# Performance work log

Measured on AMD Instinct MI355X. Metric: run time of the kernel, lower is better.

Reference implementation:

```python
import jax, jax.numpy as jnp
import numpy as np

B, DIN, DOUT, NW = 32768, 768, 768, 48
NH = NW // 3  # num_haar == num_mexican == num_morlet == 16 for NW=48
OMEGA0 = 5.0
LN_EPS = 1e-5


def setup_inputs() -> dict:
    key = jax.random.key(0)
    ks = jax.random.split(key, 6)
    x = jax.random.normal(ks[0], (B, DIN), dtype=jnp.float32)
    # kaiming-normal-ish fan_in init for linear layers, zero bias
    W = jax.random.normal(ks[1], (DOUT, DIN), dtype=jnp.float32) / np.sqrt(DIN)
    b = jnp.zeros((DOUT,), jnp.float32)
    Wp = jax.random.normal(ks[2], (NW, DIN), dtype=jnp.float32) / np.sqrt(DIN)
    bp = jnp.zeros((NW,), jnp.float32)
    Wc = jax.random.normal(ks[3], (DOUT, NW), dtype=jnp.float32) / np.sqrt(NW)
    bc = jnp.zeros((DOUT,), jnp.float32)
    # mixed-type init: per-family logspace scales / linspace translations
    scales = jnp.asarray(np.concatenate([
        np.logspace(-0.5, 0.5, NH),
        np.logspace(-0.3, 0.7, NH),
        np.logspace(-0.3, 0.7, NW - 2 * NH)]), jnp.float32)
    translations = jnp.asarray(np.concatenate([
        np.linspace(-1.5, 1.5, NH),
        np.linspace(-1.5, 1.5, NH),
        np.linspace(-1.5, 1.5, NW - 2 * NH)]), jnp.float32)
    gamma = jnp.ones((DOUT,), jnp.float32)
    beta = jnp.zeros((DOUT,), jnp.float32)
    return {"x": x, "W": W, "b": b, "Wp": Wp, "bp": bp, "Wc": Wc,
            "bc": bc, "scales": scales, "translations": translations,
            "gamma": gamma, "beta": beta}


def _wavelet_basis(s):
    # s: [B, NW] already scaled/translated; columns split by family
    dt = s.dtype
    sh = s[:, :NH]
    haar = (((sh >= 0) & (sh < 0.5)).astype(dt)
            - ((sh >= 0.5) & (sh < 1.0)).astype(dt))
    sm = s[:, NH:2 * NH]
    mexican = (1.0 - sm * sm) * jnp.exp(-0.5 * sm * sm)
    so = s[:, 2 * NH:]
    morlet = jnp.cos(OMEGA0 * so) * jnp.exp(-0.5 * so * so)
    return jnp.concatenate([haar, mexican, morlet], axis=1)


def reference(x, W, b, Wp, bp, Wc, bc, scales, translations, gamma, beta):
    direct = x @ W.T + b                              # [B, DOUT]
    wi = x @ Wp.T + bp                                # [B, NW]
    s = (wi - translations) / scales                  # [B, NW]
    wav = jax.nn.gelu(_wavelet_basis(s), approximate=False)
    wpath = wav @ Wc.T + bc                           # [B, DOUT]
    h = direct + wpath
    mu = jnp.mean(h, axis=-1, keepdims=True)
    var = jnp.mean((h - mu) ** 2, axis=-1, keepdims=True)
    return (h - mu) * jax.lax.rsqrt(var + LN_EPS) * gamma + beta
```

## Files before the change

kernel.cpp:

```cpp
#include <hip/hip_runtime.h>
#include <math.h>


#define B_SZ  32768
#define DIN   768
#define DOUT  768
#define NWAV  48

#define WF_OFF   0
#define WPH_OFF  589824
#define WPL_OFF  638976
#define WCF_OFF  688128

typedef short bf16x8 __attribute__((ext_vector_type(8)));
typedef float f32x16 __attribute__((ext_vector_type(16)));

__device__ __forceinline__ float bf2f(short u) {
    union { unsigned int i; float f; } v;
    v.i = ((unsigned int)(unsigned short)u) << 16;
    return v.f;
}
__device__ __forceinline__ short f2bf(float f) {
    union { float f; unsigned int i; } v; v.f = f;
    unsigned int r = v.i + 0x7FFFu + ((v.i >> 16) & 1u);
    return (short)(r >> 16);
}

__global__ __launch_bounds__(256) void pack_kernel(
    const float* __restrict__ W, const float* __restrict__ Wp,
    const float* __restrict__ Wc, short* __restrict__ ws)
{
    const int gw = (blockIdx.x * 256 + threadIdx.x) >> 6;
    const int L  = threadIdx.x & 63;
    const int lm = L & 31, half = L >> 5;

    if (gw < 1152) {
        const int cb = gw / 48, kb = gw % 48;
        const int row = cb * 32 + lm;
        const int k = kb * 16 + half * 8;
        bf16x8 o;
#pragma unroll
        for (int j = 0; j < 8; j++) o[j] = f2bf(W[(size_t)row * DIN + k + j]);
        *reinterpret_cast<bf16x8*>(&ws[WF_OFF + (size_t)gw * 512 + L * 8]) = o;
    } else if (gw < 1248) {
        const int t = gw - 1152;
        const int ct = t / 48, kb = t % 48;
        const int j = ct * 32 + lm;
        const int k = kb * 16 + half * 8;
        bf16x8 h, l;
#pragma unroll
        for (int jj = 0; jj < 8; jj++) {
            float v = (j < NWAV) ? Wp[(size_t)j * DIN + k + jj] : 0.f;
            const short hh = f2bf(v);
            h[jj] = hh;
            l[jj] = f2bf(v - bf2f(hh));
        }
        *reinterpret_cast<bf16x8*>(&ws[WPH_OFF + (size_t)t * 512 + L * 8]) = h;
        *reinterpret_cast<bf16x8*>(&ws[WPL_OFF + (size_t)t * 512 + L * 8]) = l;
    } else if (gw < 1320) {
        const int t = gw - 1248;
        const int cb = t / 3, kb = t % 3;
        const int row = cb * 32 + lm;
        const int k = kb * 16 + half * 8;
        bf16x8 o;
#pragma unroll
        for (int jj = 0; jj < 8; jj++) o[jj] = f2bf(Wc[(size_t)row * NWAV + k + jj]);
        *reinterpret_cast<bf16x8*>(&ws[WCF_OFF + (size_t)t * 512 + L * 8]) = o;
    }
}

__global__ __launch_bounds__(1024) void fused_kernel(
    const float* __restrict__ x, const short* __restrict__ ws,
    const float* __restrict__ Wp,
    const float* __restrict__ bp, const float* __restrict__ sc,
    const float* __restrict__ tr,
    const float* __restrict__ bb, const float* __restrict__ bc,
    const float* __restrict__ gm, const float* __restrict__ bt,
    float* __restrict__ out)
{
    __shared__ __align__(16) short xbuf[73728];
    __shared__ __align__(16) short wavL[64 * 72];
    __shared__ float redS[64 * 8], redQ[64 * 8];
    __shared__ float muA[64], rsA[64];

    short (*xh)[64 * 72] = reinterpret_cast<short (*)[64 * 72]>(&xbuf[0]);
    short (*xl)[64 * 72] = reinterpret_cast<short (*)[64 * 72]>(&xbuf[2 * 64 * 72]);
    float* wiS = reinterpret_cast<float*>(&xbuf[0]);

    const short* WF  = ws + WF_OFF;
    const short* WPH = ws + WPH_OFF;
    const short* WPL = ws + WPL_OFF;
    const short* WCF = ws + WCF_OFF;

    const int tid = threadIdx.x;
    const int r0  = blockIdx.x * 64;
    const int wv  = tid >> 6, L = tid & 63;
    const int lm  = L & 31, half = L >> 5;
    const int rg  = wv >> 3, cg = wv & 7;
    const int kq  = wv >> 2;
    const int wrg = (wv & 3) >> 1, wch = wv & 1;

    f32x16 acc[3];
#pragma unroll
    for (int ct = 0; ct < 3; ct++)
#pragma unroll
        for (int g = 0; g < 16; g++) acc[ct][g] = 0.f;
    f32x16 wacc;
#pragma unroll
    for (int g = 0; g < 16; g++) wacc[g] = 0.f;

    const int srow = tid >> 4;
    const int skc  = (tid & 15) * 4;

    {
        const float4 v = *reinterpret_cast<const float4*>(&x[(size_t)(r0 + srow) * DIN + skc]);
        const float f[4] = {v.x, v.y, v.z, v.w};
        short hh[4], ll[4];
#pragma unroll
        for (int i = 0; i < 4; i++) {
            hh[i] = f2bf(f[i]);
            ll[i] = f2bf(f[i] - bf2f(hh[i]));
        }
        *reinterpret_cast<short4*>(&xh[0][srow * 72 + skc]) = *reinterpret_cast<short4*>(hh);
        *reinterpret_cast<short4*>(&xl[0][srow * 72 + skc]) = *reinterpret_cast<short4*>(ll);
    }
    __syncthreads();

    for (int k0i = 0; k0i < 12; ++k0i) {
        const int cur = k0i & 1;
        float4 pf;
        if (k0i < 11)
            pf = *reinterpret_cast<const float4*>(&x[(size_t)(r0 + srow) * DIN + (k0i + 1) * 64 + skc]);

        const int kb0 = k0i * 4;
#pragma unroll
        for (int ks = 0; ks < 4; ++ks) {
            const bf16x8 a0 = *reinterpret_cast<bf16x8*>(&xh[cur][(rg * 32 + lm) * 72 + ks * 16 + half * 8]);
#pragma unroll
            for (int ct = 0; ct < 3; ++ct) {
                const bf16x8 b = *reinterpret_cast<const bf16x8*>(
                    &WF[((size_t)((cg * 3 + ct) * 48 + kb0 + ks)) * 512 + L * 8]);
                acc[ct] = __builtin_amdgcn_mfma_f32_32x32x16_bf16(a0, b, acc[ct], 0, 0, 0);
            }
        }
        if (k0i >= kq * 3 && k0i < kq * 3 + 3) {
#pragma unroll
            for (int ks = 0; ks < 4; ++ks) {
                const bf16x8 ah = *reinterpret_cast<bf16x8*>(&xh[cur][(wrg * 32 + lm) * 72 + ks * 16 + half * 8]);
                const bf16x8 al = *reinterpret_cast<bf16x8*>(&xl[cur][(wrg * 32 + lm) * 72 + ks * 16 + half * 8]);
                const bf16x8 bh = *reinterpret_cast<const bf16x8*>(
                    &WPH[((size_t)(wch * 48 + kb0 + ks)) * 512 + L * 8]);
                const bf16x8 bl = *reinterpret_cast<const bf16x8*>(
                    &WPL[((size_t)(wch * 48 + kb0 + ks)) * 512 + L * 8]);
                wacc = __builtin_amdgcn_mfma_f32_32x32x16_bf16(ah, bl, wacc, 0, 0, 0);
                wacc = __builtin_amdgcn_mfma_f32_32x32x16_bf16(al, bh, wacc, 0, 0, 0);
                wacc = __builtin_amdgcn_mfma_f32_32x32x16_bf16(ah, bh, wacc, 0, 0, 0);
            }
        }
        if (k0i < 11) {
            const float f[4] = {pf.x, pf.y, pf.z, pf.w};
            short hh[4], ll[4];
#pragma unroll
            for (int i = 0; i < 4; i++) {
                hh[i] = f2bf(f[i]);
                ll[i] = f2bf(f[i] - bf2f(hh[i]));
            }
            *reinterpret_cast<short4*>(&xh[1 - cur][srow * 72 + skc]) = *reinterpret_cast<short4*>(hh);
            *reinterpret_cast<short4*>(&xl[1 - cur][srow * 72 + skc]) = *reinterpret_cast<short4*>(ll);
        }
        __syncthreads();
    }

    if (kq < 2) {
#pragma unroll
        for (int g = 0; g < 16; ++g) {
            const int row = wrg * 32 + (g & 3) + 8 * (g >> 2) + 4 * half;
            wiS[(size_t)kq * 4096 + row * 64 + wch * 32 + lm] = wacc[g];
        }
    }
    __syncthreads();
    if (kq >= 2) {
#pragma unroll
        for (int g = 0; g < 16; ++g) {
            const int row = wrg * 32 + (g & 3) + 8 * (g >> 2) + 4 * half;
            wiS[(size_t)(kq - 2) * 4096 + row * 64 + wch * 32 + lm] += wacc[g];
        }
    }
    __syncthreads();

    const int j = L;
    if (j < NWAV) {
        const float bpv = bp[j], scv = sc[j], trv = tr[j];
#pragma unroll
        for (int rr = 0; rr < 4; ++rr) {
            const int row = wv * 4 + rr;
            const float wi = wiS[row * 64 + j] + wiS[4096 + row * 64 + j] + bpv;
            const float s = (wi - trv) / scv;
            float w;
            if (j < 16) {
                const float dmin = fminf(fabsf(s), fminf(fabsf(s - 0.5f), fabsf(s - 1.0f)));
                if (dmin < 2e-4f) {
                    const float* xr = &x[(size_t)(r0 + row) * DIN];
                    const float* wr = &Wp[(size_t)j * DIN];
                    double a0 = 0.0, a1 = 0.0, a2 = 0.0, a3 = 0.0;
                    for (int k = 0; k < DIN; k += 4) {
                        a0 = fma((double)xr[k + 0], (double)wr[k + 0], a0);
                        a1 = fma((double)xr[k + 1], (double)wr[k + 1], a1);
                        a2 = fma((double)xr[k + 2], (double)wr[k + 2], a2);
                        a3 = fma((double)xr[k + 3], (double)wr[k + 3], a3);
                    }
                    const double wid = ((a0 + a1) + (a2 + a3)) + (double)bpv;
                    const double sd = (wid - (double)trv) / (double)scv;
                    w = (sd >= 0.0 && sd < 0.5) ? 1.f : ((sd >= 0.5 && sd < 1.0) ? -1.f : 0.f);
                } else {
                    w = (s >= 0.f && s < 0.5f) ? 1.f : ((s >= 0.5f && s < 1.f) ? -1.f : 0.f);
                }
            } else if (j < 32) {
                w = (1.f - s * s) * expf(-0.5f * s * s);
            } else {
                w = cosf(5.f * s) * expf(-0.5f * s * s);
            }
            const float gel = 0.5f * w * (1.f + erff(w * 0.70710678118654752f));
            wavL[row * 72 + j] = f2bf(gel);
        }
    }
    __syncthreads();

#pragma unroll
    for (int ks = 0; ks < 3; ++ks) {
        const bf16x8 a0 = *reinterpret_cast<bf16x8*>(&wavL[(rg * 32 + lm) * 72 + ks * 16 + half * 8]);
#pragma unroll
        for (int ct = 0; ct < 3; ++ct) {
            const bf16x8 b = *reinterpret_cast<const bf16x8*>(
                &WCF[((size_t)((cg * 3 + ct) * 3 + ks)) * 512 + L * 8]);
            acc[ct] = __builtin_amdgcn_mfma_f32_32x32x16_bf16(a0, b, acc[ct], 0, 0, 0);
        }
    }

    float bias[3], g_[3], b_[3];
#pragma unroll
    for (int ct = 0; ct < 3; ++ct) {
        const int col = cg * 96 + ct * 32 + lm;
        bias[ct] = bb[col] + bc[col];
        g_[ct] = gm[col];
        b_[ct] = bt[col];
    }
#pragma unroll
    for (int g = 0; g < 16; ++g) {
        const float v0 = acc[0][g] + bias[0];
        const float v1 = acc[1][g] + bias[1];
        const float v2 = acc[2][g] + bias[2];
        acc[0][g] = v0; acc[1][g] = v1; acc[2][g] = v2;
        float s1 = v0 + v1 + v2;
        float s2 = v0 * v0 + v1 * v1 + v2 * v2;
        s1 += __shfl_xor(s1, 1);  s2 += __shfl_xor(s2, 1);
        s1 += __shfl_xor(s1, 2);  s2 += __shfl_xor(s2, 2);
        s1 += __shfl_xor(s1, 4);  s2 += __shfl_xor(s2, 4);
        s1 += __shfl_xor(s1, 8);  s2 += __shfl_xor(s2, 8);
        s1 += __shfl_xor(s1, 16); s2 += __shfl_xor(s2, 16);
        if (lm == 0) {
            const int row = rg * 32 + (g & 3) + 8 * (g >> 2) + 4 * half;
            redS[row * 8 + cg] = s1;
            redQ[row * 8 + cg] = s2;
        }
    }
    __syncthreads();
    if (tid < 64) {
        float S = 0.f, Q = 0.f;
#pragma unroll
        for (int i = 0; i < 8; i++) { S += redS[tid * 8 + i]; Q += redQ[tid * 8 + i]; }
        const float mu = S * (1.f / 768.f);
        const float var = Q * (1.f / 768.f) - mu * mu;
        muA[tid] = mu;
        rsA[tid] = rsqrtf(var + 1e-5f);
    }
    __syncthreads();

#pragma unroll
    for (int g = 0; g < 16; ++g) {
        const int row = rg * 32 + (g & 3) + 8 * (g >> 2) + 4 * half;
        const float mu = muA[row], rs = rsA[row];
        float* orow = &out[(size_t)(r0 + row) * DOUT + cg * 96 + lm];
#pragma unroll
        for (int ct = 0; ct < 3; ++ct) {
            orow[ct * 32] = (acc[ct][g] - mu) * rs * g_[ct] + b_[ct];
        }
    }
}

extern "C" void kernel_launch(void* const* d_in, const int* in_sizes, int n_in,
                              void* d_out, int out_size, void* d_ws, size_t ws_size,
                              hipStream_t stream)
{
    const float* x  = (const float*)d_in[0];
    const float* W  = (const float*)d_in[1];
    const float* b  = (const float*)d_in[2];
    const float* Wp = (const float*)d_in[3];
    const float* bp = (const float*)d_in[4];
    const float* Wc = (const float*)d_in[5];
    const float* bc = (const float*)d_in[6];
    const float* sc = (const float*)d_in[7];
    const float* tr = (const float*)d_in[8];
    const float* gm = (const float*)d_in[9];
    const float* bt = (const float*)d_in[10];
    float* out = (float*)d_out;
    short* ws  = (short*)d_ws;

    pack_kernel<<<dim3(330), dim3(256), 0, stream>>>(W, Wp, Wc, ws);
    fused_kernel<<<dim3(B_SZ / 64), dim3(1024), 0, stream>>>(
        x, ws, Wp, bp, sc, tr, b, bc, gm, bt, out);
}
```

Baseline: 309.3 us.

## Shrink fused block to 32 rows and 512 threads for multi-block occupancy

Halves the row tile per block from 64 to 32 rows and the block from 1024 to 512 threads, cutting shared memory from roughly 150 KB to about 32 KB. With launch bounds of (512, 4), several blocks can be resident per CU, which should hide global-load and MFMA latency better. The wavelet projection is remapped as a 4-way K split by 2 column tiles, reduced through shared memory in one pass, and the basis evaluation is spread over all threads. The cost is that each block streams the full packed weight matrix for half as many rows, doubling weight traffic from L2, plus higher register pressure under the new bounds.

```diff
diff --git a/kernel.cpp b/kernel.cpp
--- a/kernel.cpp
+++ b/kernel.cpp
@@ -69,7 +69,7 @@
     }
 }
 
-__global__ __launch_bounds__(1024) void fused_kernel(
+__global__ __launch_bounds__(512, 4) void fused_kernel(
     const float* __restrict__ x, const short* __restrict__ ws,
     const float* __restrict__ Wp,
     const float* __restrict__ bp, const float* __restrict__ sc,
@@ -78,13 +78,13 @@
     const float* __restrict__ gm, const float* __restrict__ bt,
     float* __restrict__ out)
 {
-    __shared__ __align__(16) short xbuf[73728];
-    __shared__ __align__(16) short wavL[64 * 72];
-    __shared__ float redS[64 * 8], redQ[64 * 8];
-    __shared__ float muA[64], rsA[64];
-
-    short (*xh)[64 * 72] = reinterpret_cast<short (*)[64 * 72]>(&xbuf[0]);
-    short (*xl)[64 * 72] = reinterpret_cast<short (*)[64 * 72]>(&xbuf[2 * 64 * 72]);
+    __shared__ __align__(16) short xbuf[16384];
+    __shared__ __align__(16) short wavL[32 * 72];
+    __shared__ float redS[32 * 8], redQ[32 * 8];
+    __shared__ float muA[32], rsA[32];
+
+    short (*xh)[32 * 72] = reinterpret_cast<short (*)[32 * 72]>(&xbuf[0]);
+    short (*xl)[32 * 72] = reinterpret_cast<short (*)[32 * 72]>(&xbuf[2 * 32 * 72]);
     float* wiS = reinterpret_cast<float*>(&xbuf[0]);
 
     const short* WF  = ws + WF_OFF;
@@ -93,12 +93,12 @@
     const short* WCF = ws + WCF_OFF;
 
     const int tid = threadIdx.x;
-    const int r0  = blockIdx.x * 64;
+    const int r0  = blockIdx.x * 32;
     const int wv  = tid >> 6, L = tid & 63;
     const int lm  = L & 31, half = L >> 5;
-    const int rg  = wv >> 3, cg = wv & 7;
-    const int kq  = wv >> 2;
-    const int wrg = (wv & 3) >> 1, wch = wv & 1;
+    const int cg  = wv;
+    const int kq  = wv >> 1;
+    const int wct = wv & 1;
 
     f32x16 acc[3];
 #pragma unroll
@@ -135,7 +135,7 @@
         const int kb0 = k0i * 4;
 #pragma unroll
         for (int ks = 0; ks < 4; ++ks) {
-            const bf16x8 a0 = *reinterpret_cast<bf16x8*>(&xh[cur][(rg * 32 + lm) * 72 + ks * 16 + half * 8]);
+            const bf16x8 a0 = *reinterpret_cast<bf16x8*>(&xh[cur][lm * 72 + ks * 16 + half * 8]);
 #pragma unroll
             for (int ct = 0; ct < 3; ++ct) {
                 const bf16x8 b = *reinterpret_cast<const bf16x8*>(
@@ -146,12 +146,12 @@
         if (k0i >= kq * 3 && k0i < kq * 3 + 3) {
 #pragma unroll
             for (int ks = 0; ks < 4; ++ks) {
-                const bf16x8 ah = *reinterpret_cast<bf16x8*>(&xh[cur][(wrg * 32 + lm) * 72 + ks * 16 + half * 8]);
-                const bf16x8 al = *reinterpret_cast<bf16x8*>(&xl[cur][(wrg * 32 + lm) * 72 + ks * 16 + half * 8]);
+                const bf16x8 ah = *reinterpret_cast<bf16x8*>(&xh[cur][lm * 72 + ks * 16 + half * 8]);
+                const bf16x8 al = *reinterpret_cast<bf16x8*>(&xl[cur][lm * 72 + ks * 16 + half * 8]);
                 const bf16x8 bh = *reinterpret_cast<const bf16x8*>(
-                    &WPH[((size_t)(wch * 48 + kb0 + ks)) * 512 + L * 8]);
+                    &WPH[((size_t)(wct * 48 + kb0 + ks)) * 512 + L * 8]);
                 const bf16x8 bl = *reinterpret_cast<const bf16x8*>(
-                    &WPL[((size_t)(wch * 48 + kb0 + ks)) * 512 + L * 8]);
+                    &WPL[((size_t)(wct * 48 + kb0 + ks)) * 512 + L * 8]);
                 wacc = __builtin_amdgcn_mfma_f32_32x32x16_bf16(ah, bl, wacc, 0, 0, 0);
                 wacc = __builtin_amdgcn_mfma_f32_32x32x16_bf16(al, bh, wacc, 0, 0, 0);
                 wacc = __builtin_amdgcn_mfma_f32_32x32x16_bf16(ah, bh, wacc, 0, 0, 0);
@@ -171,31 +171,24 @@
         __syncthreads();
     }
 
-    if (kq < 2) {
-#pragma unroll
-        for (int g = 0; g < 16; ++g) {
-            const int row = wrg * 32 + (g & 3) + 8 * (g >> 2) + 4 * half;
-            wiS[(size_t)kq * 4096 + row * 64 + wch * 32 + lm] = wacc[g];
-        }
-    }
-    __syncthreads();
-    if (kq >= 2) {
-#pragma unroll
-        for (int g = 0; g < 16; ++g) {
-            const int row = wrg * 32 + (g & 3) + 8 * (g >> 2) + 4 * half;
-            wiS[(size_t)(kq - 2) * 4096 + row * 64 + wch * 32 + lm] += wacc[g];
-        }
-    }
-    __syncthreads();
-
-    const int j = L;
-    if (j < NWAV) {
-        const float bpv = bp[j], scv = sc[j], trv = tr[j];
-#pragma unroll
-        for (int rr = 0; rr < 4; ++rr) {
-            const int row = wv * 4 + rr;
-            const float wi = wiS[row * 64 + j] + wiS[4096 + row * 64 + j] + bpv;
-            const float s = (wi - trv) / scv;
+#pragma unroll
+    for (int g = 0; g < 16; ++g) {
+        const int row = (g & 3) + 8 * (g >> 2) + 4 * half;
+        wiS[(size_t)kq * 2048 + row * 64 + wct * 32 + lm] = wacc[g];
+    }
+    __syncthreads();
+
+    {
+        const int row = tid >> 4;
+        wavL[row * 72 + 48 + (tid & 15)] = 0;
+        const int j0 = (tid & 15) * 3;
+#pragma unroll
+        for (int u = 0; u < 3; ++u) {
+            const int j = j0 + u;
+            const float wi = wiS[row * 64 + j] + wiS[2048 + row * 64 + j]
+                           + wiS[4096 + row * 64 + j] + wiS[6144 + row * 64 + j]
+                           + bp[j];
+            const float s = (wi - tr[j]) / sc[j];
             float w;
             if (j < 16) {
                 const float dmin = fminf(fabsf(s), fminf(fabsf(s - 0.5f), fabsf(s - 1.0f)));
@@ -209,8 +202,8 @@
                         a2 = fma((double)xr[k + 2], (double)wr[k + 2], a2);
                         a3 = fma((double)xr[k + 3], (double)wr[k + 3], a3);
                     }
-                    const double wid = ((a0 + a1) + (a2 + a3)) + (double)bpv;
-                    const double sd = (wid - (double)trv) / (double)scv;
+                    const double wid = ((a0 + a1) + (a2 + a3)) + (double)bp[j];
+                    const double sd = (wid - (double)tr[j]) / (double)sc[j];
                     w = (sd >= 0.0 && sd < 0.5) ? 1.f : ((sd >= 0.5 && sd < 1.0) ? -1.f : 0.f);
                 } else {
                     w = (s >= 0.f && s < 0.5f) ? 1.f : ((s >= 0.5f && s < 1.f) ? -1.f : 0.f);
@@ -228,7 +221,7 @@
 
 #pragma unroll
     for (int ks = 0; ks < 3; ++ks) {
-        const bf16x8 a0 = *reinterpret_cast<bf16x8*>(&wavL[(rg * 32 + lm) * 72 + ks * 16 + half * 8]);
+        const bf16x8 a0 = *reinterpret_cast<bf16x8*>(&wavL[lm * 72 + ks * 16 + half * 8]);
 #pragma unroll
         for (int ct = 0; ct < 3; ++ct) {
             const bf16x8 b = *reinterpret_cast<const bf16x8*>(
@@ -259,13 +252,13 @@
         s1 += __shfl_xor(s1, 8);  s2 += __shfl_xor(s2, 8);
         s1 += __shfl_xor(s1, 16); s2 += __shfl_xor(s2, 16);
         if (lm == 0) {
-            const int row = rg * 32 + (g & 3) + 8 * (g >> 2) + 4 * half;
+            const int row = (g & 3) + 8 * (g >> 2) + 4 * half;
             redS[row * 8 + cg] = s1;
             redQ[row * 8 + cg] = s2;
         }
     }
     __syncthreads();
-    if (tid < 64) {
+    if (tid < 32) {
         float S = 0.f, Q = 0.f;
 #pragma unroll
         for (int i = 0; i < 8; i++) { S += redS[tid * 8 + i]; Q += redQ[tid * 8 + i]; }
@@ -278,7 +271,7 @@
 
 #pragma unroll
     for (int g = 0; g < 16; ++g) {
-        const int row = rg * 32 + (g & 3) + 8 * (g >> 2) + 4 * half;
+        const int row = (g & 3) + 8 * (g >> 2) + 4 * half;
         const float mu = muA[row], rs = rsA[row];
         float* orow = &out[(size_t)(r0 + row) * DOUT + cg * 96 + lm];
 #pragma unroll
@@ -307,6 +300,6 @@
     short* ws  = (short*)d_ws;
 
     pack_kernel<<<dim3(330), dim3(256), 0, stream>>>(W, Wp, Wc, ws);
-    fused_kernel<<<dim3(B_SZ / 64), dim3(1024), 0, stream>>>(
+    fused_kernel<<<dim3(B_SZ / 32), dim3(512), 0, stream>>>(
         x, ws, Wp, bp, sc, tr, b, bc, gm, bt, out);
 }
```

Measured after the change: 316.4 us. 1.02x slower.
